# Kernel tuning notes

Measured on AMD Instinct MI355X. Metric: run time of the kernel, lower is better.

The kernel has to match this reference:

```python
import jax, jax.numpy as jnp
import numpy as np

D_G = 16384; B = 128; NNZ = 262144
CL1_F = 32; CL1_K = 6; FC1_F = 512; FC2_F = 512
NN_FC1 = 512; NN_FC2 = 256
CL4_F = 32; CL4_K = 4; FC1_G4 = 128; FC2_G4 = 64
OUT = 10; POOL1 = 8; POOL4 = 3; V4 = 10; EMB = 64
FC1FIN = CL1_F * (D_G // POOL1)        # 65536
G4OUT = CL4_F * (OUT // POOL4)         # 96
SUMFIN = FC1_F + NN_FC2 + FC2_G4 + 64  # 896


def _cheby(x, W, b, spmm, K):
    # x: [B, V, Fin]; Chebyshev recursion T_k(L) x with K-order feature stacking
    Bb, V, Fin = x.shape
    x0 = jnp.transpose(x, (1, 2, 0)).reshape(V, Fin * Bb)
    xs = [x0]
    if K > 1:
        x1 = spmm(x0)
        xs.append(x1)
        for _ in range(K - 2):
            x2 = 2.0 * spmm(x1) - x0
            xs.append(x2)
            x0, x1 = x1, x2
    X = jnp.stack(xs).reshape(K, V, Fin, Bb)
    X = jnp.transpose(X, (3, 1, 2, 0)).reshape(Bb * V, Fin * K)  # [B*V, Fin*K]
    return (X @ W.T + b).reshape(Bb, V, -1)


def _gmaxpool(x, p):
    # MaxPool1d(p) over node dim (floor truncation like torch)
    Bb, V, F = x.shape
    Vp = (V // p) * p
    return x[:, :Vp].reshape(Bb, V // p, p, F).max(axis=2)


def setup_inputs():
    key = jax.random.key(0)
    ks = jax.random.split(key, 32)
    def lin(i, fo, fi):
        return (jax.random.normal(ks[i], (fo, fi), jnp.float32) * 0.02,
                jnp.zeros((fo,), jnp.float32))
    cl1_W, cl1_b = lin(0, CL1_F, CL1_K)
    fc1_W, fc1_b = lin(1, FC1_F, FC1FIN)
    fc2_W, fc2_b = lin(2, FC2_F, FC1_F)
    fc3_W, fc3_b = lin(3, D_G, FC2_F)
    nn1_W, nn1_b = lin(4, NN_FC1, D_G)
    nn2_W, nn2_b = lin(5, NN_FC2, NN_FC1)
    cl4_W, cl4_b = lin(6, CL4_F, CL4_K * EMB)
    fcg1_W, fcg1_b = lin(7, FC1_G4, G4OUT)
    fcg2_W, fcg2_b = lin(8, FC2_G4, FC1_G4)
    nn14_W, nn14_b = lin(9, 256, V4 * EMB)
    nn24_W, nn24_b = lin(10, 64, 256)
    fcsum_W, fcsum_b = lin(11, OUT, SUMFIN)
    return {
        'x_in': jax.random.normal(ks[12], (B, D_G), jnp.float32),
        'x_embed': jax.random.normal(ks[13], (V4, EMB), jnp.float32),
        'dropout': 0,
        'L_rows': jnp.sort(jax.random.randint(ks[14], (NNZ,), 0, D_G)),
        'L_cols': jax.random.randint(ks[15], (NNZ,), 0, D_G),
        'L_vals': jax.random.normal(ks[16], (NNZ,), jnp.float32) * 0.1,
        'L_mg': jax.random.normal(ks[17], (V4, V4), jnp.float32) * 0.2,
        'cl1_W': cl1_W, 'cl1_b': cl1_b, 'fc1_W': fc1_W, 'fc1_b': fc1_b,
        'fc2_W': fc2_W, 'fc2_b': fc2_b, 'fc3_W': fc3_W, 'fc3_b': fc3_b,
        'nn1_W': nn1_W, 'nn1_b': nn1_b, 'nn2_W': nn2_W, 'nn2_b': nn2_b,
        'cl4_W': cl4_W, 'cl4_b': cl4_b, 'fcg1_W': fcg1_W, 'fcg1_b': fcg1_b,
        'fcg2_W': fcg2_W, 'fcg2_b': fcg2_b, 'nn14_W': nn14_W, 'nn14_b': nn14_b,
        'nn24_W': nn24_W, 'nn24_b': nn24_b, 'fcsum_W': fcsum_W, 'fcsum_b': fcsum_b,
    }


def reference(x_in, x_embed, dropout, L_rows, L_cols, L_vals, L_mg,
              cl1_W, cl1_b, fc1_W, fc1_b, fc2_W, fc2_b, fc3_W, fc3_b,
              nn1_W, nn1_b, nn2_W, nn2_b, cl4_W, cl4_b,
              fcg1_W, fcg1_b, fcg2_W, fcg2_b, nn14_W, nn14_b, nn24_W, nn24_b,
              fcsum_W, fcsum_b):
    Bb = x_in.shape[0]
    def spmm_L(m):  # COO SpMM: y[r] += v * m[c]
        return jax.ops.segment_sum(L_vals[:, None] * m[L_cols], L_rows,
                                   num_segments=D_G)
    # --- GCN 1 (gene graph) ---
    x = _cheby(x_in[:, :, None], cl1_W, cl1_b, spmm_L, CL1_K)
    x = jax.nn.relu(x)
    x = _gmaxpool(x, POOL1).reshape(Bb, FC1FIN)
    x_hidden_gae = jax.nn.relu(x @ fc1_W.T + fc1_b)
    # FC2_F != 0 branch; dropout p=0 is identity at this baseline
    x_decode_gae = jax.nn.relu(x_hidden_gae @ fc2_W.T + fc2_b)
    x_decode_gae = x_decode_gae @ fc3_W.T + fc3_b
    # --- NN 1 ---
    x_nn = jax.nn.relu(x_in @ nn1_W.T + nn1_b)
    x_nn = jax.nn.relu(x_nn @ nn2_W.T + nn2_b)
    # --- GCN 4 (small meta-graph, dense Laplacian) ---
    xe = jnp.broadcast_to(x_embed[None], (Bb, V4, EMB))
    xg = _cheby(xe, cl4_W, cl4_b, lambda m: L_mg @ m, CL4_K)
    xg = jax.nn.relu(xg)
    xg = _gmaxpool(xg, POOL4).reshape(Bb, G4OUT)
    xg = jax.nn.relu(xg @ fcg1_W.T + fcg1_b)
    xg = jax.nn.relu(xg @ fcg2_W.T + fcg2_b)
    # --- NN of GCN4 ---
    xn4 = xe.reshape(Bb, V4 * EMB)
    xn4 = jax.nn.relu(xn4 @ nn14_W.T + nn14_b)
    xn4 = jax.nn.relu(xn4 @ nn24_W.T + nn24_b)
    data_emb = jnp.concatenate([x_hidden_gae, x_nn, xg, xn4], axis=1)
    logp = jax.nn.log_softmax(data_emb @ fcsum_W.T + fcsum_b, axis=-1)
    return x_decode_gae, x_hidden_gae, logp
```

## Files before the change

### kernel.cpp

```cpp
#include <hip/hip_runtime.h>
#include <hip/hip_bf16.h>

#define DG 16384
#define NNZ 262144
#define BB 128

typedef __attribute__((ext_vector_type(8))) short bf16x8;
typedef __attribute__((ext_vector_type(8))) unsigned short us8;
typedef __attribute__((ext_vector_type(4))) float f32x4;
typedef __attribute__((ext_vector_type(4))) unsigned short us4;
typedef __attribute__((ext_vector_type(2))) float f32x2;

#define WS_ROWPTR 0
#define WS_XIN16  66048
#define WS_T      4260352
#define WS_XPOOL  54592000
#define WS_XB0    71369216
#define WS_XB1    75563520
#define WS_XNN1B  79757824
#define WS_DEC2   79888896
#define WS_XNN2   80019968
#define WS_HIDB   80151040
#define WS_N1     80282112
#define WS_TAIL   80283136
#define PART_NN1_OFF 0
#define PART_FC1_OFF 8388608
#define WS_NN1W16 81000448
#define WS_FC3W16 97777664
#define WS_FC2W16 114554880
#define WS_NN2W16 115079168
#define WS_FC1W16 115341312

__device__ __forceinline__ unsigned short f2bf(float f) {
  __hip_bfloat16 h = __float2bfloat16(f);
  return __builtin_bit_cast(unsigned short, h);
}
__device__ __forceinline__ float bflo(unsigned u) {
  return __builtin_bit_cast(float, u << 16);
}
__device__ __forceinline__ float bfhi(unsigned u) {
  return __builtin_bit_cast(float, u & 0xffff0000u);
}

__device__ void conv_dev(const float* __restrict__ src,
                         unsigned short* __restrict__ dst, int id) {
  #pragma unroll
  for (int j = 0; j < 8; ++j) {
    size_t el = (size_t)id * 8192 + j * 1024 + threadIdx.x * 4;
    f32x4 v = *(const f32x4*)(src + el);
    us4 o; o[0] = f2bf(v[0]); o[1] = f2bf(v[1]); o[2] = f2bf(v[2]); o[3] = f2bf(v[3]);
    *(us4*)(dst + el) = o;
  }
}

__device__ void prep_dev(const float* __restrict__ x_in, const int* __restrict__ rows,
                         int* __restrict__ rowptr, unsigned short* __restrict__ xin16,
                         int bid) {
  int idx = bid * 256 + threadIdx.x;
  if (idx <= DG) {
    int lo = 0, hi = NNZ;
    while (lo < hi) { int mid = (lo + hi) >> 1; if (rows[mid] < idx) lo = mid + 1; else hi = mid; }
    rowptr[idx] = lo;
  }
  f32x4 v = ((const f32x4*)x_in)[idx];
  us4 o; o[0] = f2bf(v[0]); o[1] = f2bf(v[1]); o[2] = f2bf(v[2]); o[3] = f2bf(v[3]);
  ((us4*)xin16)[idx] = o;
}

__device__ void transpose_dev(const float* __restrict__ x_in, float* __restrict__ T0,
                              unsigned short* __restrict__ Xb0, int id) {
  __shared__ float tl[32][33];
  int bx = id & 511, by = id >> 9;
  int v0 = bx * 32, b0 = by * 32;
  int tx = threadIdx.x & 31, ty0 = threadIdx.x >> 5;
  #pragma unroll
  for (int j = 0; j < 4; ++j) {
    int ty = ty0 + j * 8;
    tl[ty][tx] = x_in[(size_t)(b0 + ty) * DG + v0 + tx];
  }
  __syncthreads();
  #pragma unroll
  for (int j = 0; j < 4; ++j) {
    int ty = ty0 + j * 8;
    float v = tl[tx][ty];
    size_t o = (size_t)(v0 + ty) * BB + b0 + tx;
    T0[o] = v;
    Xb0[o] = f2bf(v);
  }
}

__device__ void dot4_dev(const float* __restrict__ x, const float* __restrict__ W,
                         const float* __restrict__ bias, float* __restrict__ out,
                         int K, int id) {
  int w = threadIdx.x >> 6, lane = threadIdx.x & 63;
  int o = id * 4 + w;
  float a = 0.f;
  for (int i = lane; i < K; i += 64) a += x[i] * W[(size_t)o * K + i];
  #pragma unroll
  for (int s = 32; s > 0; s >>= 1) a += __shfl_down(a, s);
  if (lane == 0) out[o] = fmaxf(a + bias[o], 0.f);
}

__device__ void g4_dev(const float* __restrict__ xe_g, const float* __restrict__ Lmg_g,
                       const float* __restrict__ W4, const float* __restrict__ b4,
                       const float* __restrict__ Wg1, const float* __restrict__ bg1,
                       const float* __restrict__ Wg2, const float* __restrict__ bg2,
                       float* __restrict__ tail) {
  __shared__ float Lm[100], Tg[4][640], xc[320], xg96[96], h1[128];
  int t = threadIdx.x;
  for (int i = t; i < 640; i += 256) Tg[0][i] = xe_g[i];
  for (int i = t; i < 100; i += 256) Lm[i] = Lmg_g[i];
  __syncthreads();
  for (int i = t; i < 640; i += 256) {
    int v = i >> 6, f = i & 63; float s = 0.f;
    #pragma unroll
    for (int u = 0; u < 10; ++u) s += Lm[v * 10 + u] * Tg[0][u * 64 + f];
    Tg[1][i] = s;
  }
  __syncthreads();
  for (int kk = 2; kk < 4; ++kk) {
    for (int i = t; i < 640; i += 256) {
      int v = i >> 6, f = i & 63; float s = 0.f;
      #pragma unroll
      for (int u = 0; u < 10; ++u) s += Lm[v * 10 + u] * Tg[kk - 1][u * 64 + f];
      Tg[kk][i] = 2.f * s - Tg[kk - 2][i];
    }
    __syncthreads();
  }
  for (int i = t; i < 320; i += 256) {
    int v = i >> 5, fo = i & 31; float s = b4[fo];
    for (int fin = 0; fin < 64; ++fin)
      #pragma unroll
      for (int k = 0; k < 4; ++k) s += Tg[k][v * 64 + fin] * W4[fo * 256 + fin * 4 + k];
    xc[i] = fmaxf(s, 0.f);
  }
  __syncthreads();
  for (int i = t; i < 96; i += 256) {
    int g = i >> 5, fo = i & 31;
    xg96[i] = fmaxf(fmaxf(xc[(3 * g) * 32 + fo], xc[(3 * g + 1) * 32 + fo]),
                    xc[(3 * g + 2) * 32 + fo]);
  }
  __syncthreads();
  for (int o = t; o < 128; o += 256) {
    float s = bg1[o];
    for (int i2 = 0; i2 < 96; ++i2) s += xg96[i2] * Wg1[o * 96 + i2];
    h1[o] = fmaxf(s, 0.f);
  }
  __syncthreads();
  for (int o = t; o < 64; o += 256) {
    float s = bg2[o];
    for (int i2 = 0; i2 < 128; ++i2) s += h1[i2] * Wg2[o * 128 + i2];
    tail[o] = fmaxf(s, 0.f);
  }
}

__global__ __launch_bounds__(256) void setup_kernel(
    const float* __restrict__ x_in, const int* __restrict__ rows,
    int* __restrict__ rowptr, unsigned short* __restrict__ xin16,
    float* __restrict__ T0, unsigned short* __restrict__ Xb0,
    const float* __restrict__ x_embed,
    const float* __restrict__ nn14_W, const float* __restrict__ nn14_b,
    float* __restrict__ n1,
    const float* __restrict__ Lmg, const float* __restrict__ W4,
    const float* __restrict__ b4, const float* __restrict__ Wg1,
    const float* __restrict__ bg1, const float* __restrict__ Wg2,
    const float* __restrict__ bg2, float* __restrict__ tail,
    const float* __restrict__ nn1_W, unsigned short* __restrict__ nn1w16,
    const float* __restrict__ fc2_W, unsigned short* __restrict__ fc2w16,
    const float* __restrict__ nn2_W, unsigned short* __restrict__ nn2w16) {
  int bid = blockIdx.x;
  if (bid < 1) g4_dev(x_embed, Lmg, W4, b4, Wg1, bg1, Wg2, bg2, tail);
  else if (bid < 65) dot4_dev(x_embed, nn14_W, nn14_b, n1, 640, bid - 1);
  else if (bid < 2113) prep_dev(x_in, rows, rowptr, xin16, bid - 65);
  else if (bid < 4161) transpose_dev(x_in, T0, Xb0, bid - 2113);
  else if (bid < 5185) conv_dev(nn1_W, nn1w16, bid - 4161);
  else if (bid < 5217) conv_dev(fc2_W, fc2w16, bid - 5185);
  else conv_dev(nn2_W, nn2w16, bid - 5217);
}

__global__ __launch_bounds__(256) void spmm3(
    const int* __restrict__ rowptr, const int* __restrict__ cols,
    const float* __restrict__ vals, const unsigned* __restrict__ X2,
    const float* __restrict__ Tprev, float* __restrict__ Tout,
    unsigned* __restrict__ Xbout, float scale,
    const float* __restrict__ csrc, unsigned short* __restrict__ cdst) {
  if (blockIdx.x >= 4096) { conv_dev(csrc, cdst, blockIdx.x - 4096); return; }
  int r = blockIdx.x * 4 + (threadIdx.x >> 6);
  int lane = threadIdx.x & 63;
  int e0 = rowptr[r], e1 = rowptr[r + 1];
  float a00 = 0.f, a01 = 0.f, a10 = 0.f, a11 = 0.f;
  int e = e0;
  for (; e + 4 <= e1; e += 4) {
    int c0 = cols[e], c1 = cols[e + 1], c2 = cols[e + 2], c3 = cols[e + 3];
    float v0 = vals[e], v1 = vals[e + 1], v2 = vals[e + 2], v3 = vals[e + 3];
    unsigned x0 = X2[c0 * 64 + lane], x1 = X2[c1 * 64 + lane];
    unsigned x2 = X2[c2 * 64 + lane], x3 = X2[c3 * 64 + lane];
    a00 += v0 * bflo(x0); a10 += v0 * bfhi(x0);
    a01 += v1 * bflo(x1); a11 += v1 * bfhi(x1);
    a00 += v2 * bflo(x2); a10 += v2 * bfhi(x2);
    a01 += v3 * bflo(x3); a11 += v3 * bfhi(x3);
  }
  for (; e < e1; ++e) {
    float v = vals[e]; unsigned x = X2[cols[e] * 64 + lane];
    a00 += v * bflo(x); a10 += v * bfhi(x);
  }
  float s0 = scale * (a00 + a01), s1 = scale * (a10 + a11);
  size_t o = (size_t)r * BB + lane * 2;
  if (Tprev) { f32x2 p = *(const f32x2*)(Tprev + o); s0 -= p[0]; s1 -= p[1]; }
  *(f32x2*)(Tout + o) = (f32x2){s0, s1};
  Xbout[(size_t)r * 64 + lane] = (unsigned)f2bf(s0) | ((unsigned)f2bf(s1) << 16);
}

__device__ void combine_dev(const float* __restrict__ Tbase, const float* __restrict__ W,
                            const float* __restrict__ bias, unsigned short* __restrict__ xpool,
                            int vp) {
  __shared__ float tile[6][8][128];
  __shared__ float Wl[192];
  __shared__ float bl[32];
  for (int i = threadIdx.x; i < 192; i += 256) Wl[i] = W[i];
  if (threadIdx.x < 32) bl[threadIdx.x] = bias[threadIdx.x];
  for (int i = threadIdx.x; i < 6144; i += 256) {
    int k = i >> 10, rem = i & 1023, j = rem >> 7, b = rem & 127;
    tile[k][j][b] = Tbase[(size_t)k * 2097152 + (size_t)(vp * 8 + j) * BB + b];
  }
  __syncthreads();
  for (int p = threadIdx.x; p < 4096; p += 256) {
    int b = p >> 5, f = p & 31;
    float m = -1e30f;
    #pragma unroll
    for (int j = 0; j < 8; ++j) {
      float s = bl[f];
      #pragma unroll
      for (int k = 0; k < 6; ++k) s += tile[k][j][b] * Wl[f * 6 + k];
      m = fmaxf(m, s);
    }
    m = fmaxf(m, 0.f);
    xpool[(size_t)b * 65536 + vp * 32 + f] = f2bf(m);
  }
}

__global__ __launch_bounds__(256) void combine_nn24(
    const float* __restrict__ Tbase, const float* __restrict__ W,
    const float* __restrict__ bias, unsigned short* __restrict__ xpool,
    const float* __restrict__ n1, const float* __restrict__ nn24_W,
    const float* __restrict__ nn24_b, float* __restrict__ tail64) {
  int bid = blockIdx.x;
  if (bid < 2048) combine_dev(Tbase, W, bias, xpool, bid);
  else dot4_dev(n1, nn24_W, nn24_b, tail64, 256, bid - 2048);
}

template<int NT, int MT>
__device__ void gemm_core2(
    unsigned short* __restrict__ Alds,
    unsigned short* __restrict__ Wlds,
    const unsigned short* __restrict__ A, const unsigned short* __restrict__ W,
    float* __restrict__ outP, unsigned short* __restrict__ outB,
    const float* __restrict__ bias, int K, int N, int Kchunk,
    int bx, int by, int row0, int relu, int partial) {
  const int LA = (MT * 16) / 32;
  const int LW = (NT * 64) / 32;
  int t = threadIdx.x, w = t >> 6, lane = t & 63, lr = lane & 15, lg = lane >> 4;
  int n0 = bx * NT * 64;
  int kbeg = by * Kchunk;
  f32x4 acc[MT][NT];
  #pragma unroll
  for (int mt = 0; mt < MT; ++mt)
    #pragma unroll
    for (int nt = 0; nt < NT; ++nt) acc[mt][nt] = (f32x4){0.f, 0.f, 0.f, 0.f};
  int rowA[LA], kkA[LA], rowW[LW], kkW[LW];
  #pragma unroll
  for (int j = 0; j < LA; ++j) { int idx = j * 256 + t; rowA[j] = idx >> 3; kkA[j] = (idx & 7) * 8; }
  #pragma unroll
  for (int j = 0; j < LW; ++j) { int idx = j * 256 + t; rowW[j] = idx >> 3; kkW[j] = (idx & 7) * 8; }
  us8 ra[LA], rw[LW];
  #pragma unroll
  for (int j = 0; j < LA; ++j)
    ra[j] = *(const us8*)(A + (size_t)(row0 + rowA[j]) * K + kbeg + kkA[j]);
  #pragma unroll
  for (int j = 0; j < LW; ++j)
    rw[j] = *(const us8*)(W + (size_t)(n0 + rowW[j]) * K + kbeg + kkW[j]);
  int stages = Kchunk >> 6;
  for (int s = 0; s < stages; ++s) {
    __syncthreads();
    #pragma unroll
    for (int j = 0; j < LA; ++j)
      *(us8*)(Alds + rowA[j] * 64 + (kkA[j] ^ ((rowA[j] & 7) << 3))) = ra[j];
    #pragma unroll
    for (int j = 0; j < LW; ++j)
      *(us8*)(Wlds + rowW[j] * 64 + (kkW[j] ^ ((rowW[j] & 7) << 3))) = rw[j];
    if (s + 1 < stages) {
      int k0 = kbeg + (s + 1) * 64;
      #pragma unroll
      for (int j = 0; j < LA; ++j)
        ra[j] = *(const us8*)(A + (size_t)(row0 + rowA[j]) * K + k0 + kkA[j]);
      #pragma unroll
      for (int j = 0; j < LW; ++j)
        rw[j] = *(const us8*)(W + (size_t)(n0 + rowW[j]) * K + k0 + kkW[j]);
    }
    __syncthreads();
    #pragma unroll
    for (int h = 0; h < 2; ++h) {
      int k32 = h * 32;
      bf16x8 bfr[NT];
      #pragma unroll
      for (int nt = 0; nt < NT; ++nt) {
        int wrow = w * NT * 16 + nt * 16 + lr;
        bfr[nt] = *(const bf16x8*)(Wlds + wrow * 64 + ((k32 + lg * 8) ^ ((wrow & 7) << 3)));
      }
      #pragma unroll
      for (int mt = 0; mt < MT; ++mt) {
        int arow = mt * 16 + lr;
        bf16x8 af = *(const bf16x8*)(Alds + arow * 64 + ((k32 + lg * 8) ^ ((arow & 7) << 3)));
        #pragma unroll
        for (int nt = 0; nt < NT; ++nt)
          acc[mt][nt] = __builtin_amdgcn_mfma_f32_16x16x32_bf16(af, bfr[nt], acc[mt][nt], 0, 0, 0);
      }
    }
  }
  if (partial) {
    float* P = outP + (size_t)by * 128 * (size_t)N;
    #pragma unroll
    for (int mt = 0; mt < MT; ++mt)
      #pragma unroll
      for (int nt = 0; nt < NT; ++nt) {
        int col = n0 + w * NT * 16 + nt * 16 + lr;
        #pragma unroll
        for (int r2 = 0; r2 < 4; ++r2) {
          int row = row0 + mt * 16 + lg * 4 + r2;
          P[(size_t)row * N + col] = acc[mt][nt][r2];
        }
      }
  } else {
    #pragma unroll
    for (int mt = 0; mt < MT; ++mt)
      #pragma unroll
      for (int nt = 0; nt < NT; ++nt) {
        int col = n0 + w * NT * 16 + nt * 16 + lr;
        float bc = bias[col];
        #pragma unroll
        for (int r2 = 0; r2 < 4; ++r2) {
          int row = row0 + mt * 16 + lg * 4 + r2;
          float v = acc[mt][nt][r2] + bc;
          if (relu) v = fmaxf(v, 0.f);
          if (outP) outP[(size_t)row * N + col] = v;
          if (outB) outB[(size_t)row * N + col] = f2bf(v);
        }
      }
  }
}

__global__ __launch_bounds__(256) void gemm_partials(
    const unsigned short* __restrict__ xin16, const unsigned short* __restrict__ nn1w16,
    const unsigned short* __restrict__ xpool, const unsigned short* __restrict__ fc1w16,
    float* __restrict__ pnn1, float* __restrict__ pfc1) {
  __shared__ unsigned short Alds[128 * 64];
  __shared__ unsigned short Wlds[128 * 64];
  int nb = blockIdx.x;
  if (nb < 128) {
    int xcd = nb & 7, q = nb >> 3, bx = q & 3, by = ((q >> 2) << 3) | xcd;
    gemm_core2<2, 8>(Alds, Wlds, xin16, nn1w16, pnn1, nullptr, nullptr,
                     16384, 512, 512, bx, by, 0, 0, 1);
  } else {
    int b = nb - 128;
    int xcd = b & 7, q = b >> 3, bx = q & 3, by = ((q >> 2) << 3) | xcd;
    gemm_core2<2, 8>(Alds, Wlds, xpool, fc1w16, pfc1, nullptr, nullptr,
                     65536, 512, 512, bx, by, 0, 0, 1);
  }
}

__global__ __launch_bounds__(256) void reduce_fused(
    const float* __restrict__ pfc1, const float* __restrict__ fc1_b,
    float* __restrict__ hidden, unsigned short* __restrict__ hidB,
    const float* __restrict__ pnn1, const float* __restrict__ nn1_b,
    unsigned short* __restrict__ xnn1b) {
  int b = blockIdx.x;
  if (b < 256) {
    int idx = b * 256 + threadIdx.x;
    float s = 0.f;
    for (int i = 0; i < 128; ++i) s += pfc1[(size_t)i * 65536 + idx];
    float v = fmaxf(s + fc1_b[idx & 511], 0.f);
    hidden[idx] = v;
    hidB[idx] = f2bf(v);
  } else {
    int idx = (b - 256) * 256 + threadIdx.x;
    float s = 0.f;
    for (int i = 0; i < 32; ++i) s += pnn1[(size_t)i * 65536 + idx];
    float v = fmaxf(s + nn1_b[idx & 511], 0.f);
    xnn1b[idx] = f2bf(v);
  }
}

__global__ __launch_bounds__(256) void fc2nn2_kernel(
    const unsigned short* __restrict__ hidB, const unsigned short* __restrict__ fc2w16,
    const float* __restrict__ fc2_b, unsigned short* __restrict__ dec2,
    const unsigned short* __restrict__ xnn1b, const unsigned short* __restrict__ nn2w16,
    const float* __restrict__ nn2_b, float* __restrict__ xnn2) {
  __shared__ unsigned short Alds[128 * 64];
  __shared__ unsigned short Wlds[64 * 64];
  int b = blockIdx.x;
  if (b < 8)
    gemm_core2<1, 8>(Alds, Wlds, hidB, fc2w16, nullptr, dec2, fc2_b,
                     512, 512, 512, b, 0, 0, 1, 0);
  else
    gemm_core2<1, 8>(Alds, Wlds, xnn1b, nn2w16, xnn2, nullptr, nn2_b,
                     512, 256, 512, b - 8, 0, 0, 1, 0);
}

__device__ void fcsum_dev(int id, const float* __restrict__ hidden,
                          const float* __restrict__ xnn2, const float* __restrict__ tail,
                          const float* __restrict__ Ws, const float* __restrict__ bs,
                          float* __restrict__ logp) {
  __shared__ float emb[4][896];
  int w = threadIdx.x >> 6, lane = threadIdx.x & 63;
  int b = id * 4 + w;
  for (int i = lane; i < 896; i += 64)
    emb[w][i] = (i < 512) ? hidden[b * 512 + i]
              : (i < 768) ? xnn2[b * 256 + (i - 512)]
                          : tail[i - 768];
  float l[10];
  #pragma unroll
  for (int o = 0; o < 10; ++o) {
    float a = 0.f;
    for (int i = lane; i < 896; i += 64) a += emb[w][i] * Ws[o * 896 + i];
    #pragma unroll
    for (int s = 32; s > 0; s >>= 1) a += __shfl_down(a, s);
    l[o] = __shfl(a, 0) + bs[o];
  }
  float m = l[0];
  #pragma unroll
  for (int o = 1; o < 10; ++o) m = fmaxf(m, l[o]);
  float sum = 0.f;
  #pragma unroll
  for (int o = 0; o < 10; ++o) sum += expf(l[o] - m);
  float lse = m + logf(sum);
  #pragma unroll
  for (int o = 0; o < 10; ++o)
    if (lane == o) logp[b * 10 + o] = l[o] - lse;
}

__global__ __launch_bounds__(256) void fc3_head(
    const unsigned short* __restrict__ dec2, const unsigned short* __restrict__ fc3w16,
    const float* __restrict__ fc3_b, float* __restrict__ out0,
    const float* __restrict__ hidden, const float* __restrict__ xnn2,
    const float* __restrict__ tail, const float* __restrict__ fcsum_W,
    const float* __restrict__ fcsum_b, float* __restrict__ logp) {
  __shared__ unsigned short Alds[64 * 64];
  __shared__ unsigned short Wlds[64 * 64];
  int b = blockIdx.x;
  if (b < 512) {
    int bx = b >> 1, my = b & 1;
    gemm_core2<1, 4>(Alds, Wlds, dec2, fc3w16, out0, nullptr, fc3_b,
                     512, 16384, 512, bx, 0, my * 64, 0, 0);
  } else {
    fcsum_dev(b - 512, hidden, xnn2, tail, fcsum_W, fcsum_b, logp);
  }
}

extern "C" void kernel_launch(void* const* d_in, const int* in_sizes, int n_in,
                              void* d_out, int out_size, void* d_ws, size_t ws_size,
                              hipStream_t stream) {
  const float* x_in    = (const float*)d_in[0];
  const float* x_embed = (const float*)d_in[1];
  const int*   L_rows  = (const int*)d_in[3];
  const int*   L_cols  = (const int*)d_in[4];
  const float* L_vals  = (const float*)d_in[5];
  const float* L_mg    = (const float*)d_in[6];
  const float* cl1_W = (const float*)d_in[7],  *cl1_b = (const float*)d_in[8];
  const float* fc1_W = (const float*)d_in[9],  *fc1_b = (const float*)d_in[10];
  const float* fc2_W = (const float*)d_in[11], *fc2_b = (const float*)d_in[12];
  const float* fc3_W = (const float*)d_in[13], *fc3_b = (const float*)d_in[14];
  const float* nn1_W = (const float*)d_in[15], *nn1_b = (const float*)d_in[16];
  const float* nn2_W = (const float*)d_in[17], *nn2_b = (const float*)d_in[18];
  const float* cl4_W = (const float*)d_in[19], *cl4_b = (const float*)d_in[20];
  const float* fcg1_W = (const float*)d_in[21], *fcg1_b = (const float*)d_in[22];
  const float* fcg2_W = (const float*)d_in[23], *fcg2_b = (const float*)d_in[24];
  const float* nn14_W = (const float*)d_in[25], *nn14_b = (const float*)d_in[26];
  const float* nn24_W = (const float*)d_in[27], *nn24_b = (const float*)d_in[28];
  const float* fcsum_W = (const float*)d_in[29], *fcsum_b = (const float*)d_in[30];

  char* ws = (char*)d_ws;
  int* rowptr = (int*)(ws + WS_ROWPTR);
  unsigned short* xin16 = (unsigned short*)(ws + WS_XIN16);
  float* T = (float*)(ws + WS_T);
  unsigned short* xpool = (unsigned short*)(ws + WS_XPOOL);
  unsigned short* Xb0 = (unsigned short*)(ws + WS_XB0);
  unsigned short* Xb1 = (unsigned short*)(ws + WS_XB1);
  unsigned short* xnn1b = (unsigned short*)(ws + WS_XNN1B);
  unsigned short* dec2 = (unsigned short*)(ws + WS_DEC2);
  float* xnn2 = (float*)(ws + WS_XNN2);
  unsigned short* hidB = (unsigned short*)(ws + WS_HIDB);
  float* n1 = (float*)(ws + WS_N1);
  float* tail = (float*)(ws + WS_TAIL);
  float* pnn1 = (float*)(ws + WS_T + PART_NN1_OFF);
  float* pfc1 = (float*)(ws + WS_T + PART_FC1_OFF);
  unsigned short* nn1w16 = (unsigned short*)(ws + WS_NN1W16);
  unsigned short* fc3w16 = (unsigned short*)(ws + WS_FC3W16);
  unsigned short* fc2w16 = (unsigned short*)(ws + WS_FC2W16);
  unsigned short* nn2w16 = (unsigned short*)(ws + WS_NN2W16);
  unsigned short* fc1w16 = (unsigned short*)(ws + WS_FC1W16);

  float* out0 = (float*)d_out;
  float* hidden = out0 + 2097152;
  float* logp = out0 + 2097152 + 65536;

  setup_kernel<<<5233, 256, 0, stream>>>(x_in, L_rows, rowptr, xin16, T, Xb0,
                                         x_embed, nn14_W, nn14_b, n1,
                                         L_mg, cl4_W, cl4_b, fcg1_W, fcg1_b,
                                         fcg2_W, fcg2_b, tail,
                                         nn1_W, nn1w16, fc2_W, fc2w16, nn2_W, nn2w16);

  spmm3<<<5120, 256, 0, stream>>>(rowptr, L_cols, L_vals, (const unsigned*)Xb0,
                                  nullptr,          T + 1 * 2097152, (unsigned*)Xb1, 1.f,
                                  fc1_W,            fc1w16);
  spmm3<<<5120, 256, 0, stream>>>(rowptr, L_cols, L_vals, (const unsigned*)Xb1,
                                  T,                T + 2 * 2097152, (unsigned*)Xb0, 2.f,
                                  fc1_W + 8388608,  fc1w16 + 8388608);
  spmm3<<<5120, 256, 0, stream>>>(rowptr, L_cols, L_vals, (const unsigned*)Xb0,
                                  T + 1 * 2097152,  T + 3 * 2097152, (unsigned*)Xb1, 2.f,
                                  fc1_W + 16777216, fc1w16 + 16777216);
  spmm3<<<5120, 256, 0, stream>>>(rowptr, L_cols, L_vals, (const unsigned*)Xb1,
                                  T + 2 * 2097152,  T + 4 * 2097152, (unsigned*)Xb0, 2.f,
                                  fc1_W + 25165824, fc1w16 + 25165824);
  spmm3<<<5120, 256, 0, stream>>>(rowptr, L_cols, L_vals, (const unsigned*)Xb0,
                                  T + 3 * 2097152,  T + 5 * 2097152, (unsigned*)Xb1, 2.f,
                                  fc3_W,            fc3w16);

  combine_nn24<<<2064, 256, 0, stream>>>(T, cl1_W, cl1_b, xpool,
                                         n1, nn24_W, nn24_b, tail + 64);

  gemm_partials<<<640, 256, 0, stream>>>(xin16, nn1w16, xpool, fc1w16, pnn1, pfc1);

  reduce_fused<<<512, 256, 0, stream>>>(pfc1, fc1_b, hidden, hidB,
                                        pnn1, nn1_b, xnn1b);

  fc2nn2_kernel<<<12, 256, 0, stream>>>(hidB, fc2w16, fc2_b, dec2,
                                        xnn1b, nn2w16, nn2_b, xnn2);

  fc3_head<<<544, 256, 0, stream>>>(dec2, fc3w16, fc3_b, out0,
                                    hidden, xnn2, tail, fcsum_W, fcsum_b, logp);
}
```

Measured before the change: 286.0 us.

## Fuse fp32-to-bf16 weight conversion into GEMM tile loads

Removes the separate weight-conversion blocks from the setup and SpMM kernels. The GEMMs now read fp32 weights directly and convert them to bf16 while staging tiles into LDS. This drops one full write and re-read of each bf16 weight copy (fc1 alone is 32M elements), at the cost of reading twice as many bytes from the fp32 weights inside the GEMMs. It also adds a missing __syncthreads in the fcsum head.

```diff
diff --git a/kernel.cpp b/kernel.cpp
--- a/kernel.cpp
+++ b/kernel.cpp
@@ -25,11 +25,6 @@
 #define WS_TAIL   80283136
 #define PART_NN1_OFF 0
 #define PART_FC1_OFF 8388608
-#define WS_NN1W16 81000448
-#define WS_FC3W16 97777664
-#define WS_FC2W16 114554880
-#define WS_NN2W16 115079168
-#define WS_FC1W16 115341312
 
 __device__ __forceinline__ unsigned short f2bf(float f) {
   __hip_bfloat16 h = __float2bfloat16(f);
@@ -40,17 +35,6 @@
 }
 __device__ __forceinline__ float bfhi(unsigned u) {
   return __builtin_bit_cast(float, u & 0xffff0000u);
-}
-
-__device__ void conv_dev(const float* __restrict__ src,
-                         unsigned short* __restrict__ dst, int id) {
-  #pragma unroll
-  for (int j = 0; j < 8; ++j) {
-    size_t el = (size_t)id * 8192 + j * 1024 + threadIdx.x * 4;
-    f32x4 v = *(const f32x4*)(src + el);
-    us4 o; o[0] = f2bf(v[0]); o[1] = f2bf(v[1]); o[2] = f2bf(v[2]); o[3] = f2bf(v[3]);
-    *(us4*)(dst + el) = o;
-  }
 }
 
 __device__ void prep_dev(const float* __restrict__ x_in, const int* __restrict__ rows,
@@ -164,27 +148,19 @@
     const float* __restrict__ Lmg, const float* __restrict__ W4,
     const float* __restrict__ b4, const float* __restrict__ Wg1,
     const float* __restrict__ bg1, const float* __restrict__ Wg2,
-    const float* __restrict__ bg2, float* __restrict__ tail,
-    const float* __restrict__ nn1_W, unsigned short* __restrict__ nn1w16,
-    const float* __restrict__ fc2_W, unsigned short* __restrict__ fc2w16,
-    const float* __restrict__ nn2_W, unsigned short* __restrict__ nn2w16) {
+    const float* __restrict__ bg2, float* __restrict__ tail) {
   int bid = blockIdx.x;
   if (bid < 1) g4_dev(x_embed, Lmg, W4, b4, Wg1, bg1, Wg2, bg2, tail);
   else if (bid < 65) dot4_dev(x_embed, nn14_W, nn14_b, n1, 640, bid - 1);
   else if (bid < 2113) prep_dev(x_in, rows, rowptr, xin16, bid - 65);
-  else if (bid < 4161) transpose_dev(x_in, T0, Xb0, bid - 2113);
-  else if (bid < 5185) conv_dev(nn1_W, nn1w16, bid - 4161);
-  else if (bid < 5217) conv_dev(fc2_W, fc2w16, bid - 5185);
-  else conv_dev(nn2_W, nn2w16, bid - 5217);
+  else transpose_dev(x_in, T0, Xb0, bid - 2113);
 }
 
 __global__ __launch_bounds__(256) void spmm3(
     const int* __restrict__ rowptr, const int* __restrict__ cols,
     const float* __restrict__ vals, const unsigned* __restrict__ X2,
     const float* __restrict__ Tprev, float* __restrict__ Tout,
-    unsigned* __restrict__ Xbout, float scale,
-    const float* __restrict__ csrc, unsigned short* __restrict__ cdst) {
-  if (blockIdx.x >= 4096) { conv_dev(csrc, cdst, blockIdx.x - 4096); return; }
+    unsigned* __restrict__ Xbout, float scale) {
   int r = blockIdx.x * 4 + (threadIdx.x >> 6);
   int lane = threadIdx.x & 63;
   int e0 = rowptr[r], e1 = rowptr[r + 1];
@@ -250,15 +226,15 @@
 }
 
 template<int NT, int MT>
-__device__ void gemm_core2(
+__device__ void gemm_core3(
     unsigned short* __restrict__ Alds,
     unsigned short* __restrict__ Wlds,
-    const unsigned short* __restrict__ A, const unsigned short* __restrict__ W,
+    const unsigned short* __restrict__ A, const float* __restrict__ W,
     float* __restrict__ outP, unsigned short* __restrict__ outB,
     const float* __restrict__ bias, int K, int N, int Kchunk,
     int bx, int by, int row0, int relu, int partial) {
-  const int LA = (MT * 16) / 32;
-  const int LW = (NT * 64) / 32;
+  const int LA = MT / 2;
+  const int LW = NT * 4;
   int t = threadIdx.x, w = t >> 6, lane = t & 63, lr = lane & 15, lg = lane >> 4;
   int n0 = bx * NT * 64;
   int kbeg = by * Kchunk;
@@ -271,14 +247,14 @@
   #pragma unroll
   for (int j = 0; j < LA; ++j) { int idx = j * 256 + t; rowA[j] = idx >> 3; kkA[j] = (idx & 7) * 8; }
   #pragma unroll
-  for (int j = 0; j < LW; ++j) { int idx = j * 256 + t; rowW[j] = idx >> 3; kkW[j] = (idx & 7) * 8; }
-  us8 ra[LA], rw[LW];
+  for (int j = 0; j < LW; ++j) { int idx = j * 256 + t; rowW[j] = idx >> 4; kkW[j] = (idx & 15) * 4; }
+  us8 ra[LA]; f32x4 rw[LW];
   #pragma unroll
   for (int j = 0; j < LA; ++j)
     ra[j] = *(const us8*)(A + (size_t)(row0 + rowA[j]) * K + kbeg + kkA[j]);
   #pragma unroll
   for (int j = 0; j < LW; ++j)
-    rw[j] = *(const us8*)(W + (size_t)(n0 + rowW[j]) * K + kbeg + kkW[j]);
+    rw[j] = *(const f32x4*)(W + (size_t)(n0 + rowW[j]) * K + kbeg + kkW[j]);
   int stages = Kchunk >> 6;
   for (int s = 0; s < stages; ++s) {
     __syncthreads();
@@ -286,8 +262,11 @@
     for (int j = 0; j < LA; ++j)
       *(us8*)(Alds + rowA[j] * 64 + (kkA[j] ^ ((rowA[j] & 7) << 3))) = ra[j];
     #pragma unroll
-    for (int j = 0; j < LW; ++j)
-      *(us8*)(Wlds + rowW[j] * 64 + (kkW[j] ^ ((rowW[j] & 7) << 3))) = rw[j];
+    for (int j = 0; j < LW; ++j) {
+      us4 o; o[0] = f2bf(rw[j][0]); o[1] = f2bf(rw[j][1]);
+      o[2] = f2bf(rw[j][2]); o[3] = f2bf(rw[j][3]);
+      *(us4*)(Wlds + rowW[j] * 64 + (kkW[j] ^ ((rowW[j] & 7) << 3))) = o;
+    }
     if (s + 1 < stages) {
       int k0 = kbeg + (s + 1) * 64;
       #pragma unroll
@@ -295,7 +274,7 @@
         ra[j] = *(const us8*)(A + (size_t)(row0 + rowA[j]) * K + k0 + kkA[j]);
       #pragma unroll
       for (int j = 0; j < LW; ++j)
-        rw[j] = *(const us8*)(W + (size_t)(n0 + rowW[j]) * K + k0 + kkW[j]);
+        rw[j] = *(const f32x4*)(W + (size_t)(n0 + rowW[j]) * K + k0 + kkW[j]);
     }
     __syncthreads();
     #pragma unroll
@@ -350,20 +329,20 @@
 }
 
 __global__ __launch_bounds__(256) void gemm_partials(
-    const unsigned short* __restrict__ xin16, const unsigned short* __restrict__ nn1w16,
-    const unsigned short* __restrict__ xpool, const unsigned short* __restrict__ fc1w16,
+    const unsigned short* __restrict__ xin16, const float* __restrict__ nn1_W,
+    const unsigned short* __restrict__ xpool, const float* __restrict__ fc1_W,
     float* __restrict__ pnn1, float* __restrict__ pfc1) {
   __shared__ unsigned short Alds[128 * 64];
   __shared__ unsigned short Wlds[128 * 64];
   int nb = blockIdx.x;
   if (nb < 128) {
     int xcd = nb & 7, q = nb >> 3, bx = q & 3, by = ((q >> 2) << 3) | xcd;
-    gemm_core2<2, 8>(Alds, Wlds, xin16, nn1w16, pnn1, nullptr, nullptr,
+    gemm_core3<2, 8>(Alds, Wlds, xin16, nn1_W, pnn1, nullptr, nullptr,
                      16384, 512, 512, bx, by, 0, 0, 1);
   } else {
     int b = nb - 128;
     int xcd = b & 7, q = b >> 3, bx = q & 3, by = ((q >> 2) << 3) | xcd;
-    gemm_core2<2, 8>(Alds, Wlds, xpool, fc1w16, pfc1, nullptr, nullptr,
+    gemm_core3<2, 8>(Alds, Wlds, xpool, fc1_W, pfc1, nullptr, nullptr,
                      65536, 512, 512, bx, by, 0, 0, 1);
   }
 }
@@ -391,18 +370,18 @@
 }
 
 __global__ __launch_bounds__(256) void fc2nn2_kernel(
-    const unsigned short* __restrict__ hidB, const unsigned short* __restrict__ fc2w16,
+    const unsigned short* __restrict__ hidB, const float* __restrict__ fc2_W,
     const float* __restrict__ fc2_b, unsigned short* __restrict__ dec2,
-    const unsigned short* __restrict__ xnn1b, const unsigned short* __restrict__ nn2w16,
+    const unsigned short* __restrict__ xnn1b, const float* __restrict__ nn2_W,
     const float* __restrict__ nn2_b, float* __restrict__ xnn2) {
   __shared__ unsigned short Alds[128 * 64];
   __shared__ unsigned short Wlds[64 * 64];
   int b = blockIdx.x;
   if (b < 8)
-    gemm_core2<1, 8>(Alds, Wlds, hidB, fc2w16, nullptr, dec2, fc2_b,
+    gemm_core3<1, 8>(Alds, Wlds, hidB, fc2_W, nullptr, dec2, fc2_b,
                      512, 512, 512, b, 0, 0, 1, 0);
   else
-    gemm_core2<1, 8>(Alds, Wlds, xnn1b, nn2w16, xnn2, nullptr, nn2_b,
+    gemm_core3<1, 8>(Alds, Wlds, xnn1b, nn2_W, xnn2, nullptr, nn2_b,
                      512, 256, 512, b - 8, 0, 0, 1, 0);
 }
 
@@ -417,6 +396,7 @@
     emb[w][i] = (i < 512) ? hidden[b * 512 + i]
               : (i < 768) ? xnn2[b * 256 + (i - 512)]
                           : tail[i - 768];
+  __syncthreads();
   float l[10];
   #pragma unroll
   for (int o = 0; o < 10; ++o) {
@@ -439,7 +419,7 @@
 }
 
 __global__ __launch_bounds__(256) void fc3_head(
-    const unsigned short* __restrict__ dec2, const unsigned short* __restrict__ fc3w16,
+    const unsigned short* __restrict__ dec2, const float* __restrict__ fc3_W,
     const float* __restrict__ fc3_b, float* __restrict__ out0,
     const float* __restrict__ hidden, const float* __restrict__ xnn2,
     const float* __restrict__ tail, const float* __restrict__ fcsum_W,
@@ -449,7 +429,7 @@
   int b = blockIdx.x;
   if (b < 512) {
     int bx = b >> 1, my = b & 1;
-    gemm_core2<1, 4>(Alds, Wlds, dec2, fc3w16, out0, nullptr, fc3_b,
+    gemm_core3<1, 4>(Alds, Wlds, dec2, fc3_W, out0, nullptr, fc3_b,
                      512, 16384, 512, bx, 0, my * 64, 0, 0);
   } else {
     fcsum_dev(b - 512, hidden, xnn2, tail, fcsum_W, fcsum_b, logp);
@@ -493,49 +473,38 @@
   float* tail = (float*)(ws + WS_TAIL);
   float* pnn1 = (float*)(ws + WS_T + PART_NN1_OFF);
   float* pfc1 = (float*)(ws + WS_T + PART_FC1_OFF);
-  unsigned short* nn1w16 = (unsigned short*)(ws + WS_NN1W16);
-  unsigned short* fc3w16 = (unsigned short*)(ws + WS_FC3W16);
-  unsigned short* fc2w16 = (unsigned short*)(ws + WS_FC2W16);
-  unsigned short* nn2w16 = (unsigned short*)(ws + WS_NN2W16);
-  unsigned short* fc1w16 = (unsigned short*)(ws + WS_FC1W16);
 
   float* out0 = (float*)d_out;
   float* hidden = out0 + 2097152;
   float* logp = out0 + 2097152 + 65536;
 
-  setup_kernel<<<5233, 256, 0, stream>>>(x_in, L_rows, rowptr, xin16, T, Xb0,
+  setup_kernel<<<4161, 256, 0, stream>>>(x_in, L_rows, rowptr, xin16, T, Xb0,
                                          x_embed, nn14_W, nn14_b, n1,
                                          L_mg, cl4_W, cl4_b, fcg1_W, fcg1_b,
-                                         fcg2_W, fcg2_b, tail,
-                                         nn1_W, nn1w16, fc2_W, fc2w16, nn2_W, nn2w16);
-
-  spmm3<<<5120, 256, 0, stream>>>(rowptr, L_cols, L_vals, (const unsigned*)Xb0,
-                                  nullptr,          T + 1 * 2097152, (unsigned*)Xb1, 1.f,
-                                  fc1_W,            fc1w16);
-  spmm3<<<5120, 256, 0, stream>>>(rowptr, L_cols, L_vals, (const unsigned*)Xb1,
-                                  T,                T + 2 * 2097152, (unsigned*)Xb0, 2.f,
-                                  fc1_W + 8388608,  fc1w16 + 8388608);
-  spmm3<<<5120, 256, 0, stream>>>(rowptr, L_cols, L_vals, (const unsigned*)Xb0,
-                                  T + 1 * 2097152,  T + 3 * 2097152, (unsigned*)Xb1, 2.f,
-                                  fc1_W + 16777216, fc1w16 + 16777216);
-  spmm3<<<5120, 256, 0, stream>>>(rowptr, L_cols, L_vals, (const unsigned*)Xb1,
-                                  T + 2 * 2097152,  T + 4 * 2097152, (unsigned*)Xb0, 2.f,
-                                  fc1_W + 25165824, fc1w16 + 25165824);
-  spmm3<<<5120, 256, 0, stream>>>(rowptr, L_cols, L_vals, (const unsigned*)Xb0,
-                                  T + 3 * 2097152,  T + 5 * 2097152, (unsigned*)Xb1, 2.f,
-                                  fc3_W,            fc3w16);
+                                         fcg2_W, fcg2_b, tail);
+
+  spmm3<<<4096, 256, 0, stream>>>(rowptr, L_cols, L_vals, (const unsigned*)Xb0,
+                                  nullptr,          T + 1 * 2097152, (unsigned*)Xb1, 1.f);
+  spmm3<<<4096, 256, 0, stream>>>(rowptr, L_cols, L_vals, (const unsigned*)Xb1,
+                                  T,                T + 2 * 2097152, (unsigned*)Xb0, 2.f);
+  spmm3<<<4096, 256, 0, stream>>>(rowptr, L_cols, L_vals, (const unsigned*)Xb0,
+                                  T + 1 * 2097152,  T + 3 * 2097152, (unsigned*)Xb1, 2.f);
+  spmm3<<<4096, 256, 0, stream>>>(rowptr, L_cols, L_vals, (const unsigned*)Xb1,
+                                  T + 2 * 2097152,  T + 4 * 2097152, (unsigned*)Xb0, 2.f);
+  spmm3<<<4096, 256, 0, stream>>>(rowptr, L_cols, L_vals, (const unsigned*)Xb0,
+                                  T + 3 * 2097152,  T + 5 * 2097152, (unsigned*)Xb1, 2.f);
 
   combine_nn24<<<2064, 256, 0, stream>>>(T, cl1_W, cl1_b, xpool,
                                          n1, nn24_W, nn24_b, tail + 64);
 
-  gemm_partials<<<640, 256, 0, stream>>>(xin16, nn1w16, xpool, fc1w16, pnn1, pfc1);
+  gemm_partials<<<640, 256, 0, stream>>>(xin16, nn1_W, xpool, fc1_W, pnn1, pfc1);
 
   reduce_fused<<<512, 256, 0, stream>>>(pfc1, fc1_b, hidden, hidB,
                                         pnn1, nn1_b, xnn1b);
 
-  fc2nn2_kernel<<<12, 256, 0, stream>>>(hidB, fc2w16, fc2_b, dec2,
-                                        xnn1b, nn2w16, nn2_b, xnn2);
-
-  fc3_head<<<544, 256, 0, stream>>>(dec2, fc3w16, fc3_b, out0,
+  fc2nn2_kernel<<<12, 256, 0, stream>>>(hidB, fc2_W, fc2_b, dec2,
+                                        xnn1b, nn2_W, nn2_b, xnn2);
+
+  fc3_head<<<544, 256, 0, stream>>>(dec2, fc3_W, fc3_b, out0,
                                     hidden, xnn2, tail, fcsum_W, fcsum_b, logp);
 }
```

Measured after the change: 282.8 us. About the same (-1.1%).
